# Kernel optimization log

Hardware: AMD Instinct MI355X
Metric: run time of the kernel (lower is better)

## Reference

```python
import jax, jax.numpy as jnp
import numpy as np
from jax import lax

N = 1024
N_I = 64
N_AV = 10
ALPHA = 0.5
RHO = 0.9
GAMMA = 1.0


def _make_params(seed=0):
    rng = np.random.RandomState(seed)
    diluition = 1.0 - N_AV / N
    W = rng.uniform(-1, 1, [N, N])
    W = W * (rng.uniform(0, 1, [N, N]) > diluition)
    eig = np.linalg.eigvals(W)
    W = (RHO * W / np.max(np.absolute(eig))).astype(np.float32)
    # N_i != 1 branch: gaussian input weights scaled by gamma
    W_in = (GAMMA * rng.randn(N_I, N)).astype(np.float32)
    return jnp.asarray(W), jnp.asarray(W_in)


def setup_inputs() -> dict:
    key = jax.random.key(0)
    Input = jax.random.normal(key, (128, N_I, 512), dtype=jnp.float32)
    W, W_in = _make_params()
    return {"Input": Input, "W": W, "W_in": W_in}


def reference(Input, W, W_in):
    # Input: [B, N_i, T] -> X: [B, N, T]
    B = Input.shape[0]
    x0 = jnp.zeros((B, W.shape[0]), dtype=Input.dtype)
    seq = jnp.transpose(Input, (2, 0, 1))  # [T, B, N_i]

    def step(x, s):
        x = (1.0 - ALPHA) * x + ALPHA * jnp.tanh(s @ W_in + x @ W)
        return x, x

    _, X = lax.scan(step, x0, seq)  # [T, B, N]
    return jnp.transpose(X, (1, 2, 0))  # [B, N, T]
```

## Files before the change

kernel.cpp:

```cpp
#include <hip/hip_runtime.h>
#include <hip/hip_fp16.h>
#include <cstdint>
#include <cstddef>

#define BB 128
#define NN 1024
#define NI 64
#define TT 512
#define MAXNNZ 16384
#define NE 28
#define TH 16
#define TCC 256

#define WS_OFFS   0u
#define WS_IDX    16384u
#define WS_VAL    65536u
#define WS_PERM   131072u
#define WS_IPERM  135168u
#define WS_XSTATE 139264u
#define WS_WINP   663552u
#define WS_EIDX2  925696u
#define WS_CNT16  983040u
#define WS_OFF16  1048576u
#define WS_U      1114112u
#define WS_U2     (WS_U + 67108864u)

__global__ __launch_bounds__(64) void k_count16(const float* __restrict__ W, int* __restrict__ cnt16) {
    int bc = blockIdx.x;
    int s = bc & 15, g = bc >> 4;
    int col = g * 64 + threadIdx.x;
    int c = 0;
    for (int q = 0; q < 64; ++q) {
        int k = s * 64 + q;
        c += (W[(size_t)k * NN + col] != 0.0f) ? 1 : 0;
    }
    cnt16[col * 16 + s] = c;
}

__global__ __launch_bounds__(1024) void k_scan3(const int* __restrict__ cnt16, int* __restrict__ offs,
                                                int* __restrict__ off16) {
    __shared__ int s[NN];
    int tid = threadIdx.x;
    int t = 0;
#pragma unroll
    for (int q = 0; q < 16; ++q) t += cnt16[tid * 16 + q];
    s[tid] = t;
    __syncthreads();
    for (int d = 1; d < NN; d <<= 1) {
        int v = (tid >= d) ? s[tid - d] : 0;
        __syncthreads();
        s[tid] += v;
        __syncthreads();
    }
    int incl = s[tid];
    offs[tid + 1] = (incl < MAXNNZ) ? incl : MAXNNZ;
    if (tid == 0) offs[0] = 0;
    int base = incl - t;
#pragma unroll
    for (int q = 0; q < 16; ++q) {
        off16[tid * 16 + q] = base;
        base += cnt16[tid * 16 + q];
    }
}

__global__ __launch_bounds__(64) void k_fill16(const float* __restrict__ W, const int* __restrict__ off16,
                                               unsigned short* __restrict__ idx, float* __restrict__ val) {
    int bc = blockIdx.x;
    int s = bc & 15, g = bc >> 4;
    int col = g * 64 + threadIdx.x;
    int p = off16[col * 16 + s];
    for (int q = 0; q < 64; ++q) {
        int k = s * 64 + q;
        float w = W[(size_t)k * NN + col];
        if (w != 0.0f) { idx[p] = (unsigned short)k; val[p] = w; ++p; }
    }
}

__global__ __launch_bounds__(1024) void k_rankchoice(const int* __restrict__ offs,
        const unsigned short* __restrict__ gidx, int* __restrict__ perm, int* __restrict__ iperm,
        unsigned short* __restrict__ eidx2) {
    __shared__ int sc[NN];
    __shared__ unsigned short rk[NN][NE];
    __shared__ unsigned short scnt[NN];
    __shared__ unsigned char ctr8[896][32];
    int n = threadIdx.x;
    sc[n] = offs[n + 1] - offs[n];
    __syncthreads();
    int myc = sc[n];
    int r = 0;
    for (int m = 0; m < NN; ++m) {
        int cm = sc[m];
        r += (cm > myc || (cm == myc && m < n)) ? 1 : 0;
    }
    perm[r] = n;
    iperm[n] = r;
    __syncthreads();
    {
        int rr = n;
        int c = perm[rr];
        int o0 = offs[c];
        int cn = offs[c + 1] - o0;
        if (cn > NE) cn = NE;
        scnt[rr] = (unsigned short)cn;
        for (int j = 0; j < cn; ++j) rk[rr][j] = (unsigned short)iperm[(int)gidx[o0 + j]];
    }
    __syncthreads();
    int tid = n;
    if (tid < 896) {
        int task = tid >> 1, h = tid & 1;
        int w = task / NE, j = task % NE;
        unsigned char* mc = &ctr8[tid][0];
        for (int b = 0; b < 32; ++b) mc[b] = 0;
        unsigned sel = 0u;
        for (int l = 0; l < 32; ++l) {
            int rr = 64 * w + 32 * h + l;
            if (j < (int)scnt[rr]) {
                int rv = (int)rk[rr][j];
                int bA = rv & 31, bB = (rv ^ (rv >> 5)) & 31;
                if (mc[bA] <= mc[bB]) mc[bA]++;
                else { sel |= (1u << l); mc[bB]++; }
            }
        }
        for (int sweep = 0; sweep < 12; ++sweep) {
            bool ch = false;
            for (int l = 0; l < 32; ++l) {
                int rr = 64 * w + 32 * h + l;
                if (j < (int)scnt[rr]) {
                    int rv = (int)rk[rr][j];
                    int bA = rv & 31, bB = (rv ^ (rv >> 5)) & 31;
                    int isB = (int)((sel >> l) & 1u);
                    int cur = isB ? bB : bA, alt = isB ? bA : bB;
                    if ((int)mc[cur] > (int)mc[alt] + 1) {
                        mc[cur]--; mc[alt]++;
                        sel ^= (1u << l);
                        ch = true;
                    }
                }
            }
            if (!ch) break;
        }
        for (int l = 0; l < 32; ++l) {
            int rr = 64 * w + 32 * h + l;
            if (j < (int)scnt[rr]) {
                int rv = (int)rk[rr][j];
                int bB = (rv ^ (rv >> 5)) & 31;
                int addr = ((sel >> l) & 1u) ? (4096 + (((rv & ~31) | bB) << 2))
                                             : (rv << 2);
                eidx2[j * NN + rr] = (unsigned short)addr;
            }
        }
        int minb = 0, minl = (int)mc[0];
        for (int b = 1; b < 32; ++b)
            if ((int)mc[b] < minl) { minl = (int)mc[b]; minb = b; }
        unsigned short pad = (unsigned short)(minb << 2);
        for (int l = 0; l < 32; ++l) {
            int rr = 64 * w + 32 * h + l;
            if (j >= (int)scnt[rr]) eidx2[j * NN + rr] = pad;
        }
    }
}

__global__ __launch_bounds__(256) void k_permwin(const float* __restrict__ Win, const int* __restrict__ perm,
                                                 float* __restrict__ Winp) {
    int idx = blockIdx.x * 256 + threadIdx.x;
    int i = idx >> 10, r = idx & 1023;
    Winp[idx] = Win[(i << 10) + perm[r]];
}

__global__ __launch_bounds__(256) void k_uproj3(const float* __restrict__ In, const float* __restrict__ Winp,
                                                __half* __restrict__ U, int t0c, int nblk) {
    int b  = blockIdx.x / nblk;
    int tq = blockIdx.x % nblk;
    int t0 = t0c + tq * 32;
    __shared__ float s[32][NI + 1];
    int tid = threadIdx.x;
    {
        int i = tid >> 2, g = tid & 3;
        const float* ip = In + ((size_t)b * NI + i) * TT + t0 + g * 8;
        float4 v0 = *(const float4*)(ip);
        float4 v1 = *(const float4*)(ip + 4);
        s[g * 8 + 0][i] = v0.x; s[g * 8 + 1][i] = v0.y;
        s[g * 8 + 2][i] = v0.z; s[g * 8 + 3][i] = v0.w;
        s[g * 8 + 4][i] = v1.x; s[g * 8 + 5][i] = v1.y;
        s[g * 8 + 6][i] = v1.z; s[g * 8 + 7][i] = v1.w;
    }
    __syncthreads();
    const float4* W4 = (const float4*)Winp;
    uint2* U2 = (uint2*)U;
    for (int th = 0; th < 2; ++th) {
        float4 acc[16];
#pragma unroll
        for (int t = 0; t < 16; ++t) acc[t] = make_float4(0.f, 0.f, 0.f, 0.f);
        for (int i = 0; i < NI; ++i) {
            float4 w = W4[(size_t)i * 256 + tid];
#pragma unroll
            for (int t = 0; t < 16; ++t) {
                float sv = s[th * 16 + t][i];
                acc[t].x = fmaf(w.x, sv, acc[t].x);
                acc[t].y = fmaf(w.y, sv, acc[t].y);
                acc[t].z = fmaf(w.z, sv, acc[t].z);
                acc[t].w = fmaf(w.w, sv, acc[t].w);
            }
        }
#pragma unroll
        for (int t = 0; t < 16; ++t) {
            __half2 h01 = __floats2half2_rn(acc[t].x, acc[t].y);
            __half2 h23 = __floats2half2_rn(acc[t].z, acc[t].w);
            uint2 pk;
            pk.x = *(unsigned int*)&h01;
            pk.y = *(unsigned int*)&h23;
            U2[((size_t)(tq * 32 + th * 16 + t) * BB + b) * 256 + tid] = pk;
        }
    }
}

__device__ __forceinline__ float fast_tanh(float z) {
    float a = fabsf(z) * 2.885390082f;
    a = fminf(a, 60.0f);
    float e = __builtin_amdgcn_exp2f(a);
    float r = 1.0f - __fdividef(2.0f, e + 1.0f);
    return z < 0.0f ? -r : r;
}

#define L28(M) \
  M(0) M(1) M(2) M(3) M(4) M(5) M(6) M(7) M(8) M(9) M(10) M(11) M(12) M(13) \
  M(14) M(15) M(16) M(17) M(18) M(19) M(20) M(21) M(22) M(23) M(24) M(25) M(26) M(27)

#define DW(i)  float w##i; int a##i;
#define IW(i)  { a##i = (int)eidx2[(i) * NN + n]; \
                 w##i = (cnt > i) ? gval[o0 + i] : 0.0f; }

#define PIN_ALL \
  asm volatile("" : "+v"(w0),"+v"(w1),"+v"(w2),"+v"(w3),"+v"(w4),"+v"(w5),"+v"(w6),"+v"(w7)); \
  asm volatile("" : "+v"(w8),"+v"(w9),"+v"(w10),"+v"(w11),"+v"(w12),"+v"(w13),"+v"(w14),"+v"(w15)); \
  asm volatile("" : "+v"(w16),"+v"(w17),"+v"(w18),"+v"(w19),"+v"(w20),"+v"(w21),"+v"(w22),"+v"(w23)); \
  asm volatile("" : "+v"(w24),"+v"(w25),"+v"(w26),"+v"(w27)); \
  asm volatile("" : "+v"(a0),"+v"(a1),"+v"(a2),"+v"(a3),"+v"(a4),"+v"(a5),"+v"(a6),"+v"(a7)); \
  asm volatile("" : "+v"(a8),"+v"(a9),"+v"(a10),"+v"(a11),"+v"(a12),"+v"(a13),"+v"(a14),"+v"(a15)); \
  asm volatile("" : "+v"(a16),"+v"(a17),"+v"(a18),"+v"(a19),"+v"(a20),"+v"(a21),"+v"(a22),"+v"(a23)); \
  asm volatile("" : "+v"(a24),"+v"(a25),"+v"(a26),"+v"(a27));

#define GRP(J, i0, i1, i2, i3) \
  if ((J) < wmax) { \
    float q0 = *(const float*)(xp + a##i0); \
    float q1 = *(const float*)(xp + a##i1); \
    float q2 = *(const float*)(xp + a##i2); \
    float q3 = *(const float*)(xp + a##i3); \
    z0 = fmaf(w##i0, q0, z0); z1 = fmaf(w##i1, q1, z1); \
    z2 = fmaf(w##i2, q2, z2); z3 = fmaf(w##i3, q3, z3); \
  }

#define GATHER_ALL \
  GRP(0, 0,1,2,3)      GRP(4, 4,5,6,7)      GRP(8, 8,9,10,11) \
  GRP(12, 12,13,14,15) GRP(16, 16,17,18,19) GRP(20, 20,21,22,23) \
  GRP(24, 24,25,26,27)

#define STEP(PH, XDST) { \
    float u = unx; \
    int tn = t + 1; tn = (tn < Tc) ? tn : (Tc - 1); \
    unx = (float)Ub[(size_t)tn * ustep]; \
    const char* xp = xb + (PH); \
    float z0 = u, z1 = 0.f, z2 = 0.f, z3 = 0.f; \
    GATHER_ALL \
    x = 0.5f * x + 0.5f * fast_tanh((z0 + z1) + (z2 + z3)); \
    XDST = x; \
    float* wb = (float*)(xb + ((PH) ^ 8192)); \
    wb[n] = x; \
    wb[NN + nB] = x; \
    __syncthreads(); \
    ++t; \
}

__global__ __launch_bounds__(1024, 4)
void k_fused(const __half* __restrict__ Uread, __half* __restrict__ Uwrite,
             const float* __restrict__ In, const float* __restrict__ Winp,
             const int* __restrict__ offs, const unsigned short* __restrict__ eidx2,
             const float* __restrict__ gval, const int* __restrict__ perm,
             float* __restrict__ out, float* __restrict__ xstate,
             int t0, int Tc) {
    __shared__ float smem[4 * 32 * 65];
    int tid = threadIdx.x;
    if (blockIdx.x < BB) {
        int b = blockIdx.x, n = tid;
        int c = perm[n];
        int nB = (n & ~31) | ((n ^ (n >> 5)) & 31);
        int o0 = offs[c];
        int cnt = offs[c + 1] - o0;
        L28(DW)
        L28(IW)
        PIN_ALL
        int wmax = cnt;
#pragma unroll
        for (int d = 1; d < 64; d <<= 1) {
            int o = __shfl_xor(wmax, d);
            wmax = wmax > o ? wmax : o;
        }
        wmax = __builtin_amdgcn_readfirstlane(wmax);

        float x = (t0 == 0) ? 0.0f : xstate[((size_t)b << 10) + n];
        smem[n] = x;
        smem[NN + nB] = x;
        __syncthreads();

        char* xb = (char*)&smem[0];
        const __half* Ub = Uread + (size_t)b * NN + n;
        const size_t ustep = (size_t)BB * NN;
        float unx = (float)Ub[0];

        for (int tb = 0; tb < Tc; tb += TH) {
            PIN_ALL
            int t = tb;
            float y0, y1, y2, y3, y4, y5, y6, y7, y8, y9, y10, y11, y12, y13, y14, y15;
            STEP(0,    y0)
            STEP(8192, y1)
            STEP(0,    y2)
            STEP(8192, y3)
            STEP(0,    y4)
            STEP(8192, y5)
            STEP(0,    y6)
            STEP(8192, y7)
            STEP(0,    y8)
            STEP(8192, y9)
            STEP(0,    y10)
            STEP(8192, y11)
            STEP(0,    y12)
            STEP(8192, y13)
            STEP(0,    y14)
            STEP(8192, y15)
            float4* op = (float4*)(out + ((size_t)b * NN + c) * TT + (size_t)(t0 + tb));
            op[0] = make_float4(y0,  y1,  y2,  y3);
            op[1] = make_float4(y4,  y5,  y6,  y7);
            op[2] = make_float4(y8,  y9,  y10, y11);
            op[3] = make_float4(y12, y13, y14, y15);
        }
        if (Tc < TT) xstate[((size_t)b << 10) + n] = x;
    } else {
        if (t0 + Tc >= TT) return;
        int b = blockIdx.x - BB;
        int sub = tid >> 8, stid = tid & 255;
        float* sg = smem + sub * 32 * 65;
        const float4* W4 = (const float4*)Winp;
        uint2* U2w = (uint2*)Uwrite;
        for (int rep = 0; rep < 2; ++rep) {
            int tq = sub * 2 + rep;
            int tg = t0 + Tc + tq * 32;
            __syncthreads();
            {
                int i = stid >> 2, g4 = stid & 3;
                const float* ip = In + ((size_t)b * NI + i) * TT + tg + g4 * 8;
                float4 v0 = *(const float4*)(ip);
                float4 v1 = *(const float4*)(ip + 4);
                sg[(g4 * 8 + 0) * 65 + i] = v0.x; sg[(g4 * 8 + 1) * 65 + i] = v0.y;
                sg[(g4 * 8 + 2) * 65 + i] = v0.z; sg[(g4 * 8 + 3) * 65 + i] = v0.w;
                sg[(g4 * 8 + 4) * 65 + i] = v1.x; sg[(g4 * 8 + 5) * 65 + i] = v1.y;
                sg[(g4 * 8 + 6) * 65 + i] = v1.z; sg[(g4 * 8 + 7) * 65 + i] = v1.w;
            }
            __syncthreads();
            for (int th = 0; th < 2; ++th) {
                float4 acc[16];
#pragma unroll
                for (int t = 0; t < 16; ++t) acc[t] = make_float4(0.f, 0.f, 0.f, 0.f);
                for (int i = 0; i < NI; ++i) {
                    float4 w = W4[(size_t)i * 256 + stid];
#pragma unroll
                    for (int t = 0; t < 16; ++t) {
                        float sv = sg[(th * 16 + t) * 65 + i];
                        acc[t].x = fmaf(w.x, sv, acc[t].x);
                        acc[t].y = fmaf(w.y, sv, acc[t].y);
                        acc[t].z = fmaf(w.z, sv, acc[t].z);
                        acc[t].w = fmaf(w.w, sv, acc[t].w);
                    }
                }
#pragma unroll
                for (int t = 0; t < 16; ++t) {
                    __half2 h01 = __floats2half2_rn(acc[t].x, acc[t].y);
                    __half2 h23 = __floats2half2_rn(acc[t].z, acc[t].w);
                    uint2 pk;
                    pk.x = *(unsigned int*)&h01;
                    pk.y = *(unsigned int*)&h23;
                    U2w[((size_t)(tq * 32 + th * 16 + t) * BB + b) * 256 + stid] = pk;
                }
            }
        }
    }
}

extern "C" void kernel_launch(void* const* d_in, const int* in_sizes, int n_in,
                              void* d_out, int out_size, void* d_ws, size_t ws_size,
                              hipStream_t stream) {
    const float* In  = (const float*)d_in[0];
    const float* W   = (const float*)d_in[1];
    const float* Win = (const float*)d_in[2];
    float* out = (float*)d_out;
    char* ws = (char*)d_ws;
    int* offs           = (int*)(ws + WS_OFFS);
    unsigned short* idx = (unsigned short*)(ws + WS_IDX);
    float* val          = (float*)(ws + WS_VAL);
    int* perm           = (int*)(ws + WS_PERM);
    int* iperm          = (int*)(ws + WS_IPERM);
    float* xstate       = (float*)(ws + WS_XSTATE);
    float* Winp         = (float*)(ws + WS_WINP);
    unsigned short* eidx2 = (unsigned short*)(ws + WS_EIDX2);
    int* cnt16          = (int*)(ws + WS_CNT16);
    int* off16          = (int*)(ws + WS_OFF16);
    __half* U0          = (__half*)(ws + WS_U);
    __half* U1          = (__half*)(ws + WS_U2);

    k_count16<<<256, 64, 0, stream>>>(W, cnt16);
    k_scan3<<<1, 1024, 0, stream>>>(cnt16, offs, off16);
    k_fill16<<<256, 64, 0, stream>>>(W, off16, idx, val);
    k_rankchoice<<<1, 1024, 0, stream>>>(offs, idx, perm, iperm, eidx2);
    k_permwin<<<256, 256, 0, stream>>>(Win, perm, Winp);

    if ((size_t)WS_U2 + (size_t)TCC * BB * NN * 2 <= ws_size) {
        k_uproj3<<<BB * (TCC / 32), 256, 0, stream>>>(In, Winp, U0, 0, TCC / 32);
        k_fused<<<2 * BB, 1024, 0, stream>>>(U0, U1, In, Winp, offs, eidx2, val, perm,
                                             out, xstate, 0, TCC);
        k_fused<<<2 * BB, 1024, 0, stream>>>(U1, U0, In, Winp, offs, eidx2, val, perm,
                                             out, xstate, TCC, TCC);
    } else {
        for (int t0 = 0; t0 < TT; t0 += TCC) {
            k_uproj3<<<BB * (TCC / 32), 256, 0, stream>>>(In, Winp, U0, t0, TCC / 32);
            k_fused<<<BB, 1024, 0, stream>>>(U0, U0, In, Winp, offs, eidx2, val, perm,
                                             out, xstate, t0, TT + TCC );
        }
    }
}
```

Baseline: 587.5 us.

## Rebalance time chunks to shrink exposed input projection and deepen U prefetch

Replaces the two equal 256-step chunks with 64/256/192-step chunks, so the non-overlapped initial input-projection kernel covers only 64 steps. The remaining projections are computed by extra blocks running alongside the recurrence kernels, and a third fused launch finishes the tail. The per-step U load is prefetched two steps ahead instead of one to hide global latency. The setup kernels are also regrouped, merging the scan with the rank computation. The cost is one more launch and unbalanced chunk sizes.

```diff
diff --git a/kernel.cpp b/kernel.cpp
--- a/kernel.cpp
+++ b/kernel.cpp
@@ -10,7 +10,9 @@
 #define MAXNNZ 16384
 #define NE 28
 #define TH 16
-#define TCC 256
+#define TC0 64
+#define TC1 256
+#define TC2 192
 
 #define WS_OFFS   0u
 #define WS_IDX    16384u
@@ -37,64 +39,55 @@
     cnt16[col * 16 + s] = c;
 }
 
-__global__ __launch_bounds__(1024) void k_scan3(const int* __restrict__ cnt16, int* __restrict__ offs,
-                                                int* __restrict__ off16) {
+__global__ __launch_bounds__(1024) void k_scanrankchoice(const int* __restrict__ cnt16,
+        const unsigned short* __restrict__ gidx, int* __restrict__ offs, int* __restrict__ off16,
+        int* __restrict__ perm, int* __restrict__ iperm, unsigned short* __restrict__ eidx2) {
     __shared__ int s[NN];
-    int tid = threadIdx.x;
-    int t = 0;
-#pragma unroll
-    for (int q = 0; q < 16; ++q) t += cnt16[tid * 16 + q];
-    s[tid] = t;
-    __syncthreads();
-    for (int d = 1; d < NN; d <<= 1) {
-        int v = (tid >= d) ? s[tid - d] : 0;
-        __syncthreads();
-        s[tid] += v;
-        __syncthreads();
-    }
-    int incl = s[tid];
-    offs[tid + 1] = (incl < MAXNNZ) ? incl : MAXNNZ;
-    if (tid == 0) offs[0] = 0;
-    int base = incl - t;
-#pragma unroll
-    for (int q = 0; q < 16; ++q) {
-        off16[tid * 16 + q] = base;
-        base += cnt16[tid * 16 + q];
-    }
-}
-
-__global__ __launch_bounds__(64) void k_fill16(const float* __restrict__ W, const int* __restrict__ off16,
-                                               unsigned short* __restrict__ idx, float* __restrict__ val) {
-    int bc = blockIdx.x;
-    int s = bc & 15, g = bc >> 4;
-    int col = g * 64 + threadIdx.x;
-    int p = off16[col * 16 + s];
-    for (int q = 0; q < 64; ++q) {
-        int k = s * 64 + q;
-        float w = W[(size_t)k * NN + col];
-        if (w != 0.0f) { idx[p] = (unsigned short)k; val[p] = w; ++p; }
-    }
-}
-
-__global__ __launch_bounds__(1024) void k_rankchoice(const int* __restrict__ offs,
-        const unsigned short* __restrict__ gidx, int* __restrict__ perm, int* __restrict__ iperm,
-        unsigned short* __restrict__ eidx2) {
-    __shared__ int sc[NN];
     __shared__ unsigned short rk[NN][NE];
     __shared__ unsigned short scnt[NN];
     __shared__ unsigned char ctr8[896][32];
     int n = threadIdx.x;
-    sc[n] = offs[n + 1] - offs[n];
-    __syncthreads();
-    int myc = sc[n];
+    int t = 0;
+#pragma unroll
+    for (int q = 0; q < 16; ++q) t += cnt16[n * 16 + q];
+    s[n] = t;
+    __syncthreads();
+    for (int d = 1; d < NN; d <<= 1) {
+        int v = (n >= d) ? s[n - d] : 0;
+        __syncthreads();
+        s[n] += v;
+        __syncthreads();
+    }
+    int incl = s[n];
+    offs[n + 1] = (incl < MAXNNZ) ? incl : MAXNNZ;
+    if (n == 0) offs[0] = 0;
+    int base = incl - t;
+#pragma unroll
+    for (int q = 0; q < 16; ++q) {
+        off16[n * 16 + q] = base;
+        base += cnt16[n * 16 + q];
+    }
+    __syncthreads();
+    int myc = offs[n + 1] - offs[n];
+    s[n] = myc;
+    __syncthreads();
     int r = 0;
     for (int m = 0; m < NN; ++m) {
-        int cm = sc[m];
+        int cm = s[m];
         r += (cm > myc || (cm == myc && m < n)) ? 1 : 0;
     }
     perm[r] = n;
     iperm[n] = r;
     __syncthreads();
+}
+
+__global__ __launch_bounds__(1024) void k_choice2(const int* __restrict__ offs,
+        const unsigned short* __restrict__ gidx, const int* __restrict__ perm,
+        const int* __restrict__ iperm, unsigned short* __restrict__ eidx2) {
+    __shared__ unsigned short rk[NN][NE];
+    __shared__ unsigned short scnt[NN];
+    __shared__ unsigned char ctr8[896][32];
+    int n = threadIdx.x;
     {
         int rr = n;
         int c = perm[rr];
@@ -157,6 +150,19 @@
             int rr = 64 * w + 32 * h + l;
             if (j >= (int)scnt[rr]) eidx2[j * NN + rr] = pad;
         }
+    }
+}
+
+__global__ __launch_bounds__(64) void k_fill16(const float* __restrict__ W, const int* __restrict__ off16,
+                                               unsigned short* __restrict__ idx, float* __restrict__ val) {
+    int bc = blockIdx.x;
+    int s = bc & 15, g = bc >> 4;
+    int col = g * 64 + threadIdx.x;
+    int p = off16[col * 16 + s];
+    for (int q = 0; q < 64; ++q) {
+        int k = s * 64 + q;
+        float w = W[(size_t)k * NN + col];
+        if (w != 0.0f) { idx[p] = (unsigned short)k; val[p] = w; ++p; }
     }
 }
 
@@ -256,9 +262,9 @@
   GRP(24, 24,25,26,27)
 
 #define STEP(PH, XDST) { \
-    float u = unx; \
-    int tn = t + 1; tn = (tn < Tc) ? tn : (Tc - 1); \
-    unx = (float)Ub[(size_t)tn * ustep]; \
+    float u = un1; un1 = un2; \
+    int tn = t + 2; tn = (tn < Tc) ? tn : (Tc - 1); \
+    un2 = (float)Ub[(size_t)tn * ustep]; \
     const char* xp = xb + (PH); \
     float z0 = u, z1 = 0.f, z2 = 0.f, z3 = 0.f; \
     GATHER_ALL \
@@ -277,7 +283,7 @@
              const int* __restrict__ offs, const unsigned short* __restrict__ eidx2,
              const float* __restrict__ gval, const int* __restrict__ perm,
              float* __restrict__ out, float* __restrict__ xstate,
-             int t0, int Tc) {
+             int t0r, int Tc, int t0u, int Tcu) {
     __shared__ float smem[4 * 32 * 65];
     int tid = threadIdx.x;
     if (blockIdx.x < BB) {
@@ -297,7 +303,7 @@
         }
         wmax = __builtin_amdgcn_readfirstlane(wmax);
 
-        float x = (t0 == 0) ? 0.0f : xstate[((size_t)b << 10) + n];
+        float x = (t0r == 0) ? 0.0f : xstate[((size_t)b << 10) + n];
         smem[n] = x;
         smem[NN + nB] = x;
         __syncthreads();
@@ -305,7 +311,8 @@
         char* xb = (char*)&smem[0];
         const __half* Ub = Uread + (size_t)b * NN + n;
         const size_t ustep = (size_t)BB * NN;
-        float unx = (float)Ub[0];
+        float un1 = (float)Ub[0];
+        float un2 = (float)Ub[(size_t)((1 < Tc) ? 1 : 0) * ustep];
 
         for (int tb = 0; tb < Tc; tb += TH) {
             PIN_ALL
@@ -327,25 +334,28 @@
             STEP(8192, y13)
             STEP(0,    y14)
             STEP(8192, y15)
-            float4* op = (float4*)(out + ((size_t)b * NN + c) * TT + (size_t)(t0 + tb));
+            float4* op = (float4*)(out + ((size_t)b * NN + c) * TT + (size_t)(t0r + tb));
             op[0] = make_float4(y0,  y1,  y2,  y3);
             op[1] = make_float4(y4,  y5,  y6,  y7);
             op[2] = make_float4(y8,  y9,  y10, y11);
             op[3] = make_float4(y12, y13, y14, y15);
         }
-        if (Tc < TT) xstate[((size_t)b << 10) + n] = x;
+        if (t0r + Tc < TT) xstate[((size_t)b << 10) + n] = x;
     } else {
-        if (t0 + Tc >= TT) return;
+        if (Tcu <= 0) return;
         int b = blockIdx.x - BB;
         int sub = tid >> 8, stid = tid & 255;
         float* sg = smem + sub * 32 * 65;
         const float4* W4 = (const float4*)Winp;
         uint2* U2w = (uint2*)Uwrite;
-        for (int rep = 0; rep < 2; ++rep) {
-            int tq = sub * 2 + rep;
-            int tg = t0 + Tc + tq * 32;
+        int ntile = Tcu >> 5;
+        int nrep = (ntile + 3) >> 2;
+        for (int rep = 0; rep < nrep; ++rep) {
+            int tq = rep * 4 + sub;
+            bool act = tq < ntile;
+            int tg = t0u + tq * 32;
             __syncthreads();
-            {
+            if (act) {
                 int i = stid >> 2, g4 = stid & 3;
                 const float* ip = In + ((size_t)b * NI + i) * TT + tg + g4 * 8;
                 float4 v0 = *(const float4*)(ip);
@@ -356,29 +366,31 @@
                 sg[(g4 * 8 + 6) * 65 + i] = v1.z; sg[(g4 * 8 + 7) * 65 + i] = v1.w;
             }
             __syncthreads();
-            for (int th = 0; th < 2; ++th) {
-                float4 acc[16];
-#pragma unroll
-                for (int t = 0; t < 16; ++t) acc[t] = make_float4(0.f, 0.f, 0.f, 0.f);
-                for (int i = 0; i < NI; ++i) {
-                    float4 w = W4[(size_t)i * 256 + stid];
+            if (act) {
+                for (int th = 0; th < 2; ++th) {
+                    float4 acc[16];
+#pragma unroll
+                    for (int t = 0; t < 16; ++t) acc[t] = make_float4(0.f, 0.f, 0.f, 0.f);
+                    for (int i = 0; i < NI; ++i) {
+                        float4 w = W4[(size_t)i * 256 + stid];
+#pragma unroll
+                        for (int t = 0; t < 16; ++t) {
+                            float sv = sg[(th * 16 + t) * 65 + i];
+                            acc[t].x = fmaf(w.x, sv, acc[t].x);
+                            acc[t].y = fmaf(w.y, sv, acc[t].y);
+                            acc[t].z = fmaf(w.z, sv, acc[t].z);
+                            acc[t].w = fmaf(w.w, sv, acc[t].w);
+                        }
+                    }
 #pragma unroll
                     for (int t = 0; t < 16; ++t) {
-                        float sv = sg[(th * 16 + t) * 65 + i];
-                        acc[t].x = fmaf(w.x, sv, acc[t].x);
-                        acc[t].y = fmaf(w.y, sv, acc[t].y);
-                        acc[t].z = fmaf(w.z, sv, acc[t].z);
-                        acc[t].w = fmaf(w.w, sv, acc[t].w);
+                        __half2 h01 = __floats2half2_rn(acc[t].x, acc[t].y);
+                        __half2 h23 = __floats2half2_rn(acc[t].z, acc[t].w);
+                        uint2 pk;
+                        pk.x = *(unsigned int*)&h01;
+                        pk.y = *(unsigned int*)&h23;
+                        U2w[((size_t)(tq * 32 + th * 16 + t) * BB + b) * 256 + stid] = pk;
                     }
-                }
-#pragma unroll
-                for (int t = 0; t < 16; ++t) {
-                    __half2 h01 = __floats2half2_rn(acc[t].x, acc[t].y);
-                    __half2 h23 = __floats2half2_rn(acc[t].z, acc[t].w);
-                    uint2 pk;
-                    pk.x = *(unsigned int*)&h01;
-                    pk.y = *(unsigned int*)&h23;
-                    U2w[((size_t)(tq * 32 + th * 16 + t) * BB + b) * 256 + stid] = pk;
                 }
             }
         }
@@ -407,22 +419,24 @@
     __half* U1          = (__half*)(ws + WS_U2);
 
     k_count16<<<256, 64, 0, stream>>>(W, cnt16);
-    k_scan3<<<1, 1024, 0, stream>>>(cnt16, offs, off16);
+    k_scanrankchoice<<<1, 1024, 0, stream>>>(cnt16, idx, offs, off16, perm, iperm, eidx2);
     k_fill16<<<256, 64, 0, stream>>>(W, off16, idx, val);
-    k_rankchoice<<<1, 1024, 0, stream>>>(offs, idx, perm, iperm, eidx2);
+    k_choice2<<<1, 1024, 0, stream>>>(offs, idx, perm, iperm, eidx2);
     k_permwin<<<256, 256, 0, stream>>>(Win, perm, Winp);
 
-    if ((size_t)WS_U2 + (size_t)TCC * BB * NN * 2 <= ws_size) {
-        k_uproj3<<<BB * (TCC / 32), 256, 0, stream>>>(In, Winp, U0, 0, TCC / 32);
+    if ((size_t)WS_U2 + (size_t)TC1 * BB * NN * 2 <= ws_size) {
+        k_uproj3<<<BB * (TC0 / 32), 256, 0, stream>>>(In, Winp, U0, 0, TC0 / 32);
         k_fused<<<2 * BB, 1024, 0, stream>>>(U0, U1, In, Winp, offs, eidx2, val, perm,
-                                             out, xstate, 0, TCC);
+                                             out, xstate, 0, TC0, TC0, TC1);
         k_fused<<<2 * BB, 1024, 0, stream>>>(U1, U0, In, Winp, offs, eidx2, val, perm,
-                                             out, xstate, TCC, TCC);
+                                             out, xstate, TC0, TC1, TC0 + TC1, TC2);
+        k_fused<<<BB, 1024, 0, stream>>>(U0, U0, In, Winp, offs, eidx2, val, perm,
+                                         out, xstate, TC0 + TC1, TC2, TT, 0);
     } else {
-        for (int t0 = 0; t0 < TT; t0 += TCC) {
-            k_uproj3<<<BB * (TCC / 32), 256, 0, stream>>>(In, Winp, U0, t0, TCC / 32);
+        for (int t0 = 0; t0 < TT; t0 += 128) {
+            k_uproj3<<<BB * 4, 256, 0, stream>>>(In, Winp, U0, t0, 4);
             k_fused<<<BB, 1024, 0, stream>>>(U0, U0, In, Winp, offs, eidx2, val, perm,
-                                             out, xstate, t0, TT + TCC );
-        }
-    }
-}
+                                             out, xstate, t0, 128, TT, 0);
+        }
+    }
+}
```

Measured after the change: 585.0 us. About the same (-0.4%).
